# Kernel optimization log

Measured on AMD Instinct MI355X. Metric: run time of the kernel, lower is better.

## Reference

```python
import jax, jax.numpy as jnp
import numpy as np

EP = 1e-4
EPMAX = 30.0
RTOL, ATOL = 1e-5, 1e-8  # torch.allclose defaults


def _safe(n):
    return jnp.where(n == 0, 1.0, n)


def _rigid_from_3(x):
    # x: (L, 3, 3) -> rot (L,3,3) rows e1,e2,e3 ; origin (L,3)
    x1, x2, x3 = x[:, 0], x[:, 1], x[:, 2]
    v1 = x3 - x2
    v2 = x1 - x2
    e1 = v1 / (jnp.linalg.norm(v1, axis=-1, keepdims=True) + 1e-3)
    u2 = v2 - e1 * jnp.einsum('ld,ld->l', e1, v2)[:, None]
    e2 = u2 / (jnp.linalg.norm(u2, axis=-1, keepdims=True) + 1e-8)
    e3 = jnp.cross(e1, e2)
    return jnp.stack([e1, e2, e3], axis=1), x2


def _merge_frames(rot, trans, ii, jj):
    # Vectorized merge_coordinate_systems over all selected pairs (ii, jj).
    O_A, O_B = trans[ii], trans[jj]          # (P,3)
    RA, RB = rot[ii], rot[jj]                # (P,3,3)
    close = jnp.all(jnp.abs(O_A - O_B) <= ATOL + RTOL * jnp.abs(O_B), axis=-1)
    d = O_B - O_A
    nd = jnp.linalg.norm(d, axis=-1)
    X_new = d / _safe(nd)[:, None]
    Z_add = RA[:, 2] + RB[:, 2]
    Z_sub = RA[:, 2] - RB[:, 2]
    na = jnp.linalg.norm(Z_add, axis=-1)
    ns = jnp.linalg.norm(Z_sub, axis=-1)
    Z_new = jnp.where((na > ns)[:, None], Z_add / _safe(na)[:, None], Z_sub / _safe(ns)[:, None])
    Y_new = jnp.cross(Z_new, X_new)
    nan_bad = jnp.any(jnp.isnan(Y_new), axis=-1)
    flip = jnp.einsum('pd,pd->p', jnp.cross(X_new, Y_new), Z_new) < 0
    Y_new = jnp.where(flip[:, None], -Y_new, Y_new)
    R_new = jnp.stack([X_new, Y_new, Z_new], axis=1)  # (P,3,3)
    O_new = 0.5 * (O_A + O_B)
    bad = close | (nd == 0) | (na == 0) | (ns == 0) | nan_bad
    R_out = jnp.where(bad[:, None, None], RA, R_new)
    O_out = jnp.where(bad[:, None], O_A, O_new)
    return jnp.concatenate([rot, R_out], axis=0), jnp.concatenate([trans, O_out], axis=0)


def _frame_transform(points, rot, tran):
    # points: (N,3); rot: (F,3,3); tran: (F,3) -> (N,F,3)
    diff = points[:, None, :] - tran[None, :, :]
    return jnp.einsum('nfd,fed->nfe', diff, rot)


def setup_inputs():
    key = jax.random.key(0)
    k0, k1, k2, k3 = jax.random.split(key, 4)
    L = 1024
    coor = 5.0 * jax.random.normal(k0, (L, 3, 3), jnp.float32)
    # valid orthonormal frames from random points
    rot, _ = _rigid_from_3(5.0 * jax.random.normal(k1, (L, 3, 3), jnp.float32))
    trans = 5.0 * jax.random.normal(k2, (L, 3), jnp.float32)
    target = 5.0 * jax.random.normal(k3, (L, 3, 3), jnp.float32)
    idx = np.arange(L)
    band = idx[None, :] - idx[:, None]
    matrix = ((band > 0) & (band <= 8)).astype(np.int32)  # ~8k contact pairs
    return {"coor": coor, "rot": rot, "trans": trans, "target": target,
            "matrix": jnp.asarray(matrix)}


def reference(coor, rot, trans, target, matrix):
    m = np.asarray(matrix)
    ii_np, jj_np = np.nonzero(np.triu(m, 1) == 1)
    ii, jj = jnp.asarray(ii_np), jnp.asarray(jj_np)
    p_rot, p_tran = _merge_frames(rot, trans, ii, jj)
    pred_x2 = _frame_transform(coor.reshape(-1, 3), p_rot, p_tran)   # (N,F,3)
    t_rot0, t_tran0 = _rigid_from_3(target)
    t_rot, t_tran = _merge_frames(t_rot0, t_tran0, ii, jj)
    tx = _frame_transform(target.reshape(-1, 3), t_rot, t_tran)     # (N,F,3)
    errmap = jnp.sqrt(jnp.sum((pred_x2 - tx) ** 2 + EP, axis=-1))
    return jnp.mean(jnp.minimum(errmap, EPMAX))
```

## Files before the change

kernel.cpp:

```cpp
#include <hip/hip_runtime.h>

#define EPV    0.0001f
#define EPMAXV 30.0f
#define RTOLV  1e-5f
#define ATOLV  1e-8f
#define CHUNK  64
#define NPART  1024


__global__ void k_rowcnt(const int* __restrict__ m, int L, unsigned int* __restrict__ rowcnt) {
    int i = blockIdx.x * 4 + (threadIdx.x >> 6);
    if (i >= L) return;
    int lane = threadIdx.x & 63;
    const int* row = m + (size_t)i * L;
    unsigned int c = 0;
    for (int j0 = 0; j0 < L; j0 += 64) {
        int j = j0 + lane;
        bool v = (j < L) && (j > i) && (row[j] == 1);
        unsigned long long b = __ballot(v);
        c += (unsigned int)__popcll(b);
    }
    if (lane == 0) rowcnt[i] = c;
}

__global__ void k_scan(const unsigned int* __restrict__ rowcnt, int L,
                       unsigned int* __restrict__ rowoff, unsigned int* __restrict__ count) {
    __shared__ unsigned int s[256];
    unsigned int carry = 0;
    for (int base = 0; base < L; base += 256) {
        int idx = base + threadIdx.x;
        unsigned int v = (idx < L) ? rowcnt[idx] : 0u;
        s[threadIdx.x] = v;
        __syncthreads();
        for (int off = 1; off < 256; off <<= 1) {
            unsigned int t = (threadIdx.x >= (unsigned)off) ? s[threadIdx.x - off] : 0u;
            __syncthreads();
            s[threadIdx.x] += t;
            __syncthreads();
        }
        if (idx < L) rowoff[idx] = carry + s[threadIdx.x] - v;
        carry += s[255];
        __syncthreads();
    }
    if (threadIdx.x == 0) *count = carry;
}

__global__ void k_fill(const int* __restrict__ m, int L, const unsigned int* __restrict__ rowoff,
                       int2* __restrict__ pairs, int cap) {
    int i = blockIdx.x * 4 + (threadIdx.x >> 6);
    if (i >= L) return;
    int lane = threadIdx.x & 63;
    const int* row = m + (size_t)i * L;
    unsigned int base = rowoff[i];
    unsigned long long lt = (lane == 0) ? 0ull : ((1ull << lane) - 1ull);
    for (int j0 = 0; j0 < L; j0 += 64) {
        int j = j0 + lane;
        bool v = (j < L) && (j > i) && (row[j] == 1);
        unsigned long long b = __ballot(v);
        if (v) {
            unsigned int pos = base + (unsigned int)__popcll(b & lt);
            if (pos < (unsigned int)cap) pairs[pos] = make_int2(i, j);
        }
        base += (unsigned int)__popcll(b);
    }
}

__global__ void k_base(const float* __restrict__ rot, const float* __restrict__ trans,
                       const float* __restrict__ target, int L,
                       float* __restrict__ pF, float* __restrict__ tF) {
    int l = blockIdx.x * 256 + threadIdx.x;
    if (l >= L) return;
    float* pf = pF + l * 12;
#pragma unroll
    for (int k = 0; k < 9; k++) pf[k] = rot[l * 9 + k];
    pf[9]  = trans[l * 3 + 0];
    pf[10] = trans[l * 3 + 1];
    pf[11] = trans[l * 3 + 2];
    const float* tg = target + l * 9;
    float x1x = tg[0], x1y = tg[1], x1z = tg[2];
    float x2x = tg[3], x2y = tg[4], x2z = tg[5];
    float x3x = tg[6], x3y = tg[7], x3z = tg[8];
    float v1x = x3x - x2x, v1y = x3y - x2y, v1z = x3z - x2z;
    float v2x = x1x - x2x, v2y = x1y - x2y, v2z = x1z - x2z;
    float n1 = sqrtf(v1x * v1x + v1y * v1y + v1z * v1z) + 0.001f;
    float e1x = v1x / n1, e1y = v1y / n1, e1z = v1z / n1;
    float c = e1x * v2x + e1y * v2y + e1z * v2z;
    float u2x = v2x - c * e1x, u2y = v2y - c * e1y, u2z = v2z - c * e1z;
    float n2 = sqrtf(u2x * u2x + u2y * u2y + u2z * u2z) + 1e-8f;
    float e2x = u2x / n2, e2y = u2y / n2, e2z = u2z / n2;
    float e3x = e1y * e2z - e1z * e2y;
    float e3y = e1z * e2x - e1x * e2z;
    float e3z = e1x * e2y - e1y * e2x;
    float* tf = tF + l * 12;
    tf[0] = e1x; tf[1] = e1y; tf[2] = e1z;
    tf[3] = e2x; tf[4] = e2y; tf[5] = e2z;
    tf[6] = e3x; tf[7] = e3y; tf[8] = e3z;
    tf[9] = x2x; tf[10] = x2y; tf[11] = x2z;
}

__device__ inline void merge_frames(const float* __restrict__ A, const float* __restrict__ B,
                                    float* __restrict__ out) {
    const float* RA = A; const float* OA = A + 9;
    const float* RB = B; const float* OB = B + 9;
    bool close = (fabsf(OA[0] - OB[0]) <= ATOLV + RTOLV * fabsf(OB[0])) &&
                 (fabsf(OA[1] - OB[1]) <= ATOLV + RTOLV * fabsf(OB[1])) &&
                 (fabsf(OA[2] - OB[2]) <= ATOLV + RTOLV * fabsf(OB[2]));
    float d0 = OB[0] - OA[0], d1 = OB[1] - OA[1], d2 = OB[2] - OA[2];
    float nd = sqrtf(d0 * d0 + d1 * d1 + d2 * d2);
    float nds = (nd == 0.f) ? 1.f : nd;
    float X0 = d0 / nds, X1 = d1 / nds, X2 = d2 / nds;
    float Za0 = RA[6] + RB[6], Za1 = RA[7] + RB[7], Za2 = RA[8] + RB[8];
    float Zs0 = RA[6] - RB[6], Zs1 = RA[7] - RB[7], Zs2 = RA[8] - RB[8];
    float na = sqrtf(Za0 * Za0 + Za1 * Za1 + Za2 * Za2);
    float ns = sqrtf(Zs0 * Zs0 + Zs1 * Zs1 + Zs2 * Zs2);
    float nas = (na == 0.f) ? 1.f : na;
    float nss = (ns == 0.f) ? 1.f : ns;
    float Z0, Z1, Z2;
    if (na > ns) { Z0 = Za0 / nas; Z1 = Za1 / nas; Z2 = Za2 / nas; }
    else         { Z0 = Zs0 / nss; Z1 = Zs1 / nss; Z2 = Zs2 / nss; }
    float Y0 = Z1 * X2 - Z2 * X1;
    float Y1 = Z2 * X0 - Z0 * X2;
    float Y2 = Z0 * X1 - Z1 * X0;
    bool nanbad = (Y0 != Y0) || (Y1 != Y1) || (Y2 != Y2);
    float C0 = X1 * Y2 - X2 * Y1;
    float C1 = X2 * Y0 - X0 * Y2;
    float C2 = X0 * Y1 - X1 * Y0;
    float dotv = C0 * Z0 + C1 * Z1 + C2 * Z2;
    if (dotv < 0.f) { Y0 = -Y0; Y1 = -Y1; Y2 = -Y2; }
    bool bad = close || (nd == 0.f) || (na == 0.f) || (ns == 0.f) || nanbad;
    if (bad) {
#pragma unroll
        for (int k = 0; k < 12; k++) out[k] = A[k];
    } else {
        out[0] = X0; out[1] = X1; out[2] = X2;
        out[3] = Y0; out[4] = Y1; out[5] = Y2;
        out[6] = Z0; out[7] = Z1; out[8] = Z2;
        out[9]  = 0.5f * (OA[0] + OB[0]);
        out[10] = 0.5f * (OA[1] + OB[1]);
        out[11] = 0.5f * (OA[2] + OB[2]);
    }
}

__global__ void k_merge(const int2* __restrict__ pairs, const unsigned int* __restrict__ count,
                        int cap, int L, float* __restrict__ pF, float* __restrict__ tF) {
    int p = blockIdx.x * 256 + threadIdx.x;
    unsigned int cnt = *count;
    if (cnt > (unsigned int)cap) cnt = (unsigned int)cap;
    if (p >= (int)cnt) return;
    int2 ij = pairs[p];
    merge_frames(pF + ij.x * 12, pF + ij.y * 12, pF + (size_t)(L + p) * 12);
    merge_frames(tF + ij.x * 12, tF + ij.y * 12, tF + (size_t)(L + p) * 12);
}

__global__ __launch_bounds__(256)
void k_main(const float* __restrict__ coor, const float* __restrict__ target,
            const float* __restrict__ pF, const float* __restrict__ tF,
            const unsigned int* __restrict__ count, int cap, int L, int Npts,
            double* __restrict__ partials) {
    __shared__ float4 sC[CHUNK];
    __shared__ float4 sT[CHUNK];
    __shared__ float sRed[4];
    unsigned int cnt = *count;
    if (cnt > (unsigned int)cap) cnt = (unsigned int)cap;
    int F = L + (int)cnt;
    int nfb = (F + 255) >> 8;
    int nyc = (Npts + CHUNK - 1) / CHUNK;
    int total = nfb * nyc;
    float a0 = 0.f, a1 = 0.f;

    for (int chunk = blockIdx.x; chunk < total; chunk += gridDim.x) {
        int fb = chunk % nfb;
        int yc = chunk / nfb;
        int n0 = yc * CHUNK;
        int npts = Npts - n0; if (npts > CHUNK) npts = CHUNK;
        __syncthreads();
        for (int idx = threadIdx.x; idx < npts; idx += 256) {
            int g = (n0 + idx) * 3;
            sC[idx] = make_float4(coor[g], coor[g + 1], coor[g + 2], 0.f);
            sT[idx] = make_float4(target[g], target[g + 1], target[g + 2], 0.f);
        }
        __syncthreads();
        int f = fb * 256 + threadIdx.x;
        if (f >= F) continue;

        const float4* pf4 = (const float4*)(pF + (size_t)f * 12);
        const float4* tf4 = (const float4*)(tF + (size_t)f * 12);
        float4 p0 = pf4[0], p1 = pf4[1], p2 = pf4[2];
        float4 t0 = tf4[0], t1 = tf4[1], t2 = tf4[2];
        float P00 = p0.x, P01 = p0.y, P02 = p0.z;
        float P10 = p0.w, P11 = p1.x, P12 = p1.y;
        float P20 = p1.z, P21 = p1.w, P22 = p2.x;
        float tPx = p2.y, tPy = p2.z, tPz = p2.w;
        float T00 = t0.x, T01 = t0.y, T02 = t0.z;
        float T10 = t0.w, T11 = t1.x, T12 = t1.y;
        float T20 = t1.z, T21 = t1.w, T22 = t2.x;
        float tTx = t2.y, tTy = t2.z, tTz = t2.w;
        float kx = T00 * tTx + T01 * tTy + T02 * tTz - (P00 * tPx + P01 * tPy + P02 * tPz);
        float ky = T10 * tTx + T11 * tTy + T12 * tTz - (P10 * tPx + P11 * tPy + P12 * tPz);
        float kz = T20 * tTx + T21 * tTy + T22 * tTz - (P20 * tPx + P21 * tPy + P22 * tPz);
        float N00 = -T00, N01 = -T01, N02 = -T02;
        float N10 = -T10, N11 = -T11, N12 = -T12;
        float N20 = -T20, N21 = -T21, N22 = -T22;

#pragma unroll 4
        for (int n = 0; n < npts; n++) {
            float4 c = sC[n];
            float4 t = sT[n];
            float ux = kx + P00 * c.x + P01 * c.y + P02 * c.z
                          + N00 * t.x + N01 * t.y + N02 * t.z;
            float uy = ky + P10 * c.x + P11 * c.y + P12 * c.z
                          + N10 * t.x + N11 * t.y + N12 * t.z;
            float uz = kz + P20 * c.x + P21 * c.y + P22 * c.z
                          + N20 * t.x + N21 * t.y + N22 * t.z;
            float s = ux * ux + uy * uy + uz * uz + 3.0f * EPV;
            float r = fminf(sqrtf(s), EPMAXV);
            if (n & 1) a1 += r; else a0 += r;
        }
    }

    float a = a0 + a1;
#pragma unroll
    for (int off = 32; off > 0; off >>= 1) a += __shfl_down(a, off, 64);
    int lane = threadIdx.x & 63, wv = threadIdx.x >> 6;
    if (lane == 0) sRed[wv] = a;
    __syncthreads();
    if (threadIdx.x == 0)
        partials[blockIdx.x] = (double)(sRed[0] + sRed[1] + sRed[2] + sRed[3]);
}

__global__ void k_final(const double* __restrict__ partials, int npart,
                        const unsigned int* __restrict__ count, int cap,
                        int L, int Npts, float* __restrict__ out) {
    __shared__ double sR[4];
    double d = 0.0;
    for (int i = threadIdx.x; i < npart; i += 256) d += partials[i];
#pragma unroll
    for (int off = 32; off > 0; off >>= 1) d += __shfl_down(d, off, 64);
    int lane = threadIdx.x & 63, wv = threadIdx.x >> 6;
    if (lane == 0) sR[wv] = d;
    __syncthreads();
    if (threadIdx.x == 0) {
        double tot = sR[0] + sR[1] + sR[2] + sR[3];
        unsigned int cnt = *count;
        if (cnt > (unsigned int)cap) cnt = (unsigned int)cap;
        double F = (double)(L + (int)cnt);
        out[0] = (float)(tot / ((double)Npts * F));
    }
}

extern "C" void kernel_launch(void* const* d_in, const int* in_sizes, int n_in,
                              void* d_out, int out_size, void* d_ws, size_t ws_size,
                              hipStream_t stream) {
    const float* coor   = (const float*)d_in[0];
    const float* rot    = (const float*)d_in[1];
    const float* trans  = (const float*)d_in[2];
    const float* target = (const float*)d_in[3];
    const int*   matrix = (const int*)d_in[4];
    int L    = in_sizes[2] / 3;
    int Npts = 3 * L;

    char* ws = (char*)d_ws;
    size_t off = 16;
    unsigned int* count  = (unsigned int*)(ws + 8);
    unsigned int* rowcnt = (unsigned int*)(ws + off); off += 4 * (size_t)L;
    unsigned int* rowoff = (unsigned int*)(ws + off); off += 4 * (size_t)L;
    off = (off + 15) & ~(size_t)15;
    double* partials = (double*)(ws + off); off += 8 * (size_t)NPART;
    off = (off + 15) & ~(size_t)15;
    long cap_ws = ((long)ws_size - (long)off - 96L * (long)L) / 104;
    long capl = cap_ws < 32768 ? cap_ws : 32768;
    if (capl < 0) capl = 0;
    int cap = (int)(capl & ~1L);
    int2*  pairs = (int2*)(ws + off);
    float* pF = (float*)(ws + off + (size_t)cap * 8);
    float* tF = pF + (size_t)(L + cap) * 12;

    int nrb = (L + 3) / 4;
    k_rowcnt<<<nrb, 256, 0, stream>>>(matrix, L, rowcnt);
    k_base<<<(L + 255) / 256, 256, 0, stream>>>(rot, trans, target, L, pF, tF);
    k_scan<<<1, 256, 0, stream>>>(rowcnt, L, rowoff, count);
    k_fill<<<nrb, 256, 0, stream>>>(matrix, L, rowoff, pairs, cap);
    if (cap > 0)
        k_merge<<<(cap + 255) / 256, 256, 0, stream>>>(pairs, count, cap, L, pF, tF);
    k_main<<<NPART, 256, 0, stream>>>(coor, target, pF, tF, count, cap, L, Npts, partials);
    k_final<<<1, 256, 0, stream>>>(partials, NPART, count, cap, L, Npts, (float*)d_out);
}
```

Before: 122.5 us.

## Fuse pair extraction, scan and merge into fewer kernels; double main partials

Merges row counting with base frame setup into one launch, replaces the single-block scan with per-row prefix sums computed by each wave, and merges frames directly during pair enumeration instead of writing a pairs buffer. This cuts the launch count from seven to four and removes the pairs round trip. In exchange, each row redundantly sums up to L row counts, and merge work becomes divergent inside waves. NPART is also doubled for the main reduction grid.

```diff
diff --git a/kernel.cpp b/kernel.cpp
--- a/kernel.cpp
+++ b/kernel.cpp
@@ -2,73 +2,30 @@
 
 #define EPV    0.0001f
 #define EPMAXV 30.0f
-#define RTOLV  1e-5f
-#define ATOLV  1e-8f
 #define CHUNK  64
-#define NPART  1024
-
-
-__global__ void k_rowcnt(const int* __restrict__ m, int L, unsigned int* __restrict__ rowcnt) {
-    int i = blockIdx.x * 4 + (threadIdx.x >> 6);
-    if (i >= L) return;
-    int lane = threadIdx.x & 63;
-    const int* row = m + (size_t)i * L;
-    unsigned int c = 0;
-    for (int j0 = 0; j0 < L; j0 += 64) {
-        int j = j0 + lane;
-        bool v = (j < L) && (j > i) && (row[j] == 1);
-        unsigned long long b = __ballot(v);
-        c += (unsigned int)__popcll(b);
-    }
-    if (lane == 0) rowcnt[i] = c;
-}
-
-__global__ void k_scan(const unsigned int* __restrict__ rowcnt, int L,
-                       unsigned int* __restrict__ rowoff, unsigned int* __restrict__ count) {
-    __shared__ unsigned int s[256];
-    unsigned int carry = 0;
-    for (int base = 0; base < L; base += 256) {
-        int idx = base + threadIdx.x;
-        unsigned int v = (idx < L) ? rowcnt[idx] : 0u;
-        s[threadIdx.x] = v;
-        __syncthreads();
-        for (int off = 1; off < 256; off <<= 1) {
-            unsigned int t = (threadIdx.x >= (unsigned)off) ? s[threadIdx.x - off] : 0u;
-            __syncthreads();
-            s[threadIdx.x] += t;
-            __syncthreads();
-        }
-        if (idx < L) rowoff[idx] = carry + s[threadIdx.x] - v;
-        carry += s[255];
-        __syncthreads();
-    }
-    if (threadIdx.x == 0) *count = carry;
-}
-
-__global__ void k_fill(const int* __restrict__ m, int L, const unsigned int* __restrict__ rowoff,
-                       int2* __restrict__ pairs, int cap) {
-    int i = blockIdx.x * 4 + (threadIdx.x >> 6);
-    if (i >= L) return;
-    int lane = threadIdx.x & 63;
-    const int* row = m + (size_t)i * L;
-    unsigned int base = rowoff[i];
-    unsigned long long lt = (lane == 0) ? 0ull : ((1ull << lane) - 1ull);
-    for (int j0 = 0; j0 < L; j0 += 64) {
-        int j = j0 + lane;
-        bool v = (j < L) && (j > i) && (row[j] == 1);
-        unsigned long long b = __ballot(v);
-        if (v) {
-            unsigned int pos = base + (unsigned int)__popcll(b & lt);
-            if (pos < (unsigned int)cap) pairs[pos] = make_int2(i, j);
-        }
-        base += (unsigned int)__popcll(b);
-    }
-}
-
-__global__ void k_base(const float* __restrict__ rot, const float* __restrict__ trans,
-                       const float* __restrict__ target, int L,
+#define NPART  2048
+
+
+__global__ void k_prep(const int* __restrict__ m, int L, unsigned int* __restrict__ rowcnt,
+                       const float* __restrict__ rot, const float* __restrict__ trans,
+                       const float* __restrict__ target, int nrb,
                        float* __restrict__ pF, float* __restrict__ tF) {
-    int l = blockIdx.x * 256 + threadIdx.x;
+    if ((int)blockIdx.x < nrb) {
+        int i = blockIdx.x * 4 + (threadIdx.x >> 6);
+        if (i >= L) return;
+        int lane = threadIdx.x & 63;
+        const int* row = m + (size_t)i * L;
+        unsigned int c = 0;
+        for (int j0 = 0; j0 < L; j0 += 64) {
+            int j = j0 + lane;
+            bool v = (j < L) && (j > i) && (row[j] == 1);
+            unsigned long long b = __ballot(v);
+            c += (unsigned int)__popcll(b);
+        }
+        if (lane == 0) rowcnt[i] = c;
+        return;
+    }
+    int l = ((int)blockIdx.x - nrb) * 256 + threadIdx.x;
     if (l >= L) return;
     float* pf = pF + l * 12;
 #pragma unroll
@@ -97,6 +54,9 @@
     tf[6] = e3x; tf[7] = e3y; tf[8] = e3z;
     tf[9] = x2x; tf[10] = x2y; tf[11] = x2z;
 }
+
+#define RTOLV  1e-5f
+#define ATOLV  1e-8f
 
 __device__ inline void merge_frames(const float* __restrict__ A, const float* __restrict__ B,
                                     float* __restrict__ out) {
@@ -141,15 +101,43 @@
     }
 }
 
-__global__ void k_merge(const int2* __restrict__ pairs, const unsigned int* __restrict__ count,
-                        int cap, int L, float* __restrict__ pF, float* __restrict__ tF) {
-    int p = blockIdx.x * 256 + threadIdx.x;
-    unsigned int cnt = *count;
-    if (cnt > (unsigned int)cap) cnt = (unsigned int)cap;
-    if (p >= (int)cnt) return;
-    int2 ij = pairs[p];
-    merge_frames(pF + ij.x * 12, pF + ij.y * 12, pF + (size_t)(L + p) * 12);
-    merge_frames(tF + ij.x * 12, tF + ij.y * 12, tF + (size_t)(L + p) * 12);
+__global__ void k_fillmerge(const int* __restrict__ m, int L,
+                            const unsigned int* __restrict__ rowcnt,
+                            unsigned int* __restrict__ count, int cap,
+                            float* __restrict__ pF, float* __restrict__ tF) {
+    int i = blockIdx.x * 4 + (threadIdx.x >> 6);
+    int lane = threadIdx.x & 63;
+
+    if (blockIdx.x == 0 && (threadIdx.x >> 6) == 0) {
+        unsigned int t = 0;
+        for (int r = lane; r < L; r += 64) t += rowcnt[r];
+#pragma unroll
+        for (int off = 1; off < 64; off <<= 1) t += __shfl_xor(t, off, 64);
+        if (lane == 0) *count = t;
+    }
+    if (i >= L) return;
+
+    unsigned int p = 0;
+    for (int r = lane; r < i; r += 64) p += rowcnt[r];
+#pragma unroll
+    for (int off = 1; off < 64; off <<= 1) p += __shfl_xor(p, off, 64);
+    unsigned int base = p;
+
+    const int* row = m + (size_t)i * L;
+    unsigned long long lt = (lane == 0) ? 0ull : ((1ull << lane) - 1ull);
+    for (int j0 = 0; j0 < L; j0 += 64) {
+        int j = j0 + lane;
+        bool v = (j < L) && (j > i) && (row[j] == 1);
+        unsigned long long b = __ballot(v);
+        if (v) {
+            unsigned int pos = base + (unsigned int)__popcll(b & lt);
+            if (pos < (unsigned int)cap) {
+                merge_frames(pF + i * 12, pF + j * 12, pF + (size_t)(L + pos) * 12);
+                merge_frames(tF + i * 12, tF + j * 12, tF + (size_t)(L + pos) * 12);
+            }
+        }
+        base += (unsigned int)__popcll(b);
+    }
 }
 
 __global__ __launch_bounds__(256)
@@ -261,27 +249,23 @@
 
     char* ws = (char*)d_ws;
     size_t off = 16;
-    unsigned int* count  = (unsigned int*)(ws + 8);
+    unsigned int* count  = (unsigned int*)ws;
     unsigned int* rowcnt = (unsigned int*)(ws + off); off += 4 * (size_t)L;
-    unsigned int* rowoff = (unsigned int*)(ws + off); off += 4 * (size_t)L;
     off = (off + 15) & ~(size_t)15;
     double* partials = (double*)(ws + off); off += 8 * (size_t)NPART;
     off = (off + 15) & ~(size_t)15;
-    long cap_ws = ((long)ws_size - (long)off - 96L * (long)L) / 104;
+    long cap_ws = ((long)ws_size - (long)off - 96L * (long)L) / 96;
     long capl = cap_ws < 32768 ? cap_ws : 32768;
     if (capl < 0) capl = 0;
     int cap = (int)(capl & ~1L);
-    int2*  pairs = (int2*)(ws + off);
-    float* pF = (float*)(ws + off + (size_t)cap * 8);
+    float* pF = (float*)(ws + off);
     float* tF = pF + (size_t)(L + cap) * 12;
 
-    int nrb = (L + 3) / 4;
-    k_rowcnt<<<nrb, 256, 0, stream>>>(matrix, L, rowcnt);
-    k_base<<<(L + 255) / 256, 256, 0, stream>>>(rot, trans, target, L, pF, tF);
-    k_scan<<<1, 256, 0, stream>>>(rowcnt, L, rowoff, count);
-    k_fill<<<nrb, 256, 0, stream>>>(matrix, L, rowoff, pairs, cap);
-    if (cap > 0)
-        k_merge<<<(cap + 255) / 256, 256, 0, stream>>>(pairs, count, cap, L, pF, tF);
+    int nrb   = (L + 3) / 4;
+    int nbase = (L + 255) / 256;
+    k_prep<<<nrb + nbase, 256, 0, stream>>>(matrix, L, rowcnt, rot, trans, target,
+                                            nrb, pF, tF);
+    k_fillmerge<<<nrb, 256, 0, stream>>>(matrix, L, rowcnt, count, cap, pF, tF);
     k_main<<<NPART, 256, 0, stream>>>(coor, target, pF, tF, count, cap, L, Npts, partials);
     k_final<<<1, 256, 0, stream>>>(partials, NPART, count, cap, L, Npts, (float*)d_out);
 }
```

Result: faster. 114.8 us (-6.2%).
